# Performance work log

Measured on AMD Instinct MI355X. Metric: run time of the kernel, lower is better.

## Reference

```python
import jax, jax.numpy as jnp
import numpy as np

N = 100000      # nodes
E = 1600000     # edges (avg degree 16)
G = 2000        # graphs
D_IN = 4        # node_in_dim
H = 128         # hidden_dim
L = 3           # num_layers


def setup_inputs() -> dict:
    key = jax.random.key(0)
    ks = jax.random.split(key, 16)
    si = 1.0 / np.sqrt(D_IN)
    sh = 1.0 / np.sqrt(H)
    inp = {
        "x": jax.random.normal(ks[0], (N, D_IN), jnp.float32),
        "edge_index": jax.random.randint(ks[1], (2, E), 0, N, dtype=jnp.int32),
        "batch": jnp.sort(jax.random.randint(ks[2], (N,), 0, G, dtype=jnp.int32)),
        "proj_w": jax.random.normal(ks[3], (D_IN, H), jnp.float32) * si,
        "proj_b": jnp.zeros((H,), jnp.float32),
        "conv_w1": jax.random.normal(ks[4], (L, H, H), jnp.float32) * sh,
        "conv_b1": jnp.zeros((L, H), jnp.float32),
        "conv_w2": jax.random.normal(ks[5], (L, H, H), jnp.float32) * sh,
        "conv_b2": jnp.zeros((L, H), jnp.float32),
        "shared_w": jax.random.normal(ks[6], (H, H), jnp.float32) * sh,
        "shared_b": jnp.zeros((H,), jnp.float32),
        "e_w": jax.random.normal(ks[7], (H, 1), jnp.float32) * sh,
        "e_b": jnp.zeros((1,), jnp.float32),
        "d_w": jax.random.normal(ks[8], (H, 1), jnp.float32) * sh,
        "d_b": jnp.zeros((1,), jnp.float32),
    }
    return inp


def reference(x, edge_index, batch, proj_w, proj_b, conv_w1, conv_b1,
              conv_w2, conv_b2, shared_w, shared_b, e_w, e_b, d_w, d_b):
    src, dst = edge_index[0], edge_index[1]
    # input projection: [N, D_IN] -> [N, H]
    h = x @ proj_w + proj_b
    # GIN layers: h' = relu(MLP((1+eps)*h + sum_{j->i} h_j)), eps = 0
    for l in range(L):
        agg = jax.ops.segment_sum(h[src], dst, num_segments=N)  # scatter-add
        m = h + agg
        m = jax.nn.relu(m @ conv_w1[l] + conv_b1[l]) @ conv_w2[l] + conv_b2[l]
        h = jax.nn.relu(m)
    # global mean pool over graphs: [N, H] -> [G, H]
    sums = jax.ops.segment_sum(h, batch, num_segments=G)
    cnt = jax.ops.segment_sum(jnp.ones((N,), h.dtype), batch, num_segments=G)
    g = sums / jnp.maximum(cnt, 1.0)[:, None]
    # shared head (dropout inactive in eval)
    g = jax.nn.relu(g @ shared_w + shared_b)
    energy = (g @ e_w + e_b).reshape(-1)
    dipole = (g @ d_w + d_b).reshape(-1)
    return (energy, dipole)
```

## Files before the change

### kernel.cpp

```cpp
#include <hip/hip_runtime.h>
#include <hip/hip_bf16.h>

#define H 128
#define REGSZ 512
#define PCHUNK 4096

typedef short short8 __attribute__((ext_vector_type(8)));
typedef float f32x4 __attribute__((ext_vector_type(4)));

__device__ __forceinline__ float bf2f(unsigned short u) {
    union { unsigned int i; float f; } c; c.i = ((unsigned int)u) << 16; return c.f;
}
__device__ __forceinline__ unsigned short f2bf(float f) {
    return __builtin_bit_cast(unsigned short, __float2bfloat16(f));
}
__device__ __forceinline__ uint2 pack_fp8x8(const float* f) {
    unsigned int lo = 0, hi = 0;
    lo = __builtin_amdgcn_cvt_pk_fp8_f32(f[0], f[1], lo, 0);
    lo = __builtin_amdgcn_cvt_pk_fp8_f32(f[2], f[3], lo, 1);
    hi = __builtin_amdgcn_cvt_pk_fp8_f32(f[4], f[5], hi, 0);
    hi = __builtin_amdgcn_cvt_pk_fp8_f32(f[6], f[7], hi, 1);
    return make_uint2(lo, hi);
}
__device__ __forceinline__ void unpack_fp8x8(uint2 v, float* f) {
    f[0] = __builtin_amdgcn_cvt_f32_fp8(v.x, 0);
    f[1] = __builtin_amdgcn_cvt_f32_fp8(v.x, 1);
    f[2] = __builtin_amdgcn_cvt_f32_fp8(v.x, 2);
    f[3] = __builtin_amdgcn_cvt_f32_fp8(v.x, 3);
    f[4] = __builtin_amdgcn_cvt_f32_fp8(v.y, 0);
    f[5] = __builtin_amdgcn_cvt_f32_fp8(v.y, 1);
    f[6] = __builtin_amdgcn_cvt_f32_fp8(v.y, 2);
    f[7] = __builtin_amdgcn_cvt_f32_fp8(v.y, 3);
}

__global__ void proj_prep_kernel(const float* __restrict__ x, const float* __restrict__ pw,
                                 const float* __restrict__ pb, unsigned char* __restrict__ h8,
                                 int N, const float* __restrict__ cw1, const float* __restrict__ cw2,
                                 unsigned short* __restrict__ wt, int wtotal, int wblocks) {
    int b = blockIdx.x;
    int tid = threadIdx.x;
    if (b < wblocks) {
        int idx = b * 256 + tid;
        if (idx < wtotal) {
            int m = idx >> 14;
            int o = (idx >> 7) & 127;
            int i = idx & 127;
            const float* srcp = (m < 3) ? (cw1 + (size_t)m * H * H) : (cw2 + (size_t)(m - 3) * H * H);
            wt[idx] = f2bf(srcp[i * H + o]);
        }
        return;
    }
    int t2 = (b - wblocks) * 256 + tid;
    if (t2 >= N * 16) return;
    int i = t2 >> 4, c = (t2 & 15) * 8;
    float4 xv = *(const float4*)&x[i * 4];
    float acc[8];
#pragma unroll
    for (int j = 0; j < 8; ++j)
        acc[j] = pb[c + j] + xv.x * pw[0 * H + c + j] + xv.y * pw[1 * H + c + j]
               + xv.z * pw[2 * H + c + j] + xv.w * pw[3 * H + c + j];
    *(uint2*)&h8[(size_t)i * H + c] = pack_fp8x8(acc);
}

__global__ __launch_bounds__(256) void partition_kernel(
    const int* __restrict__ src, const int* __restrict__ dst,
    int* __restrict__ rcnt, int* __restrict__ bucket,
    int E, int nreg, int cap) {
    __shared__ int hcnt[256];
    __shared__ int hbase[256];
    int tid = threadIdx.x;
    hcnt[tid] = 0;
    __syncthreads();
    int e0 = blockIdx.x * PCHUNK;
    int e1 = min(e0 + PCHUNK, E);
    int nv = (e1 - e0) >> 2;
    const int4* dst4 = (const int4*)(dst + e0);
    const int4* src4 = (const int4*)(src + e0);
    for (int k = tid; k < nv; k += 256) {
        int4 d = dst4[k];
        atomicAdd(&hcnt[d.x >> 9], 1);
        atomicAdd(&hcnt[d.y >> 9], 1);
        atomicAdd(&hcnt[d.z >> 9], 1);
        atomicAdd(&hcnt[d.w >> 9], 1);
    }
    for (int e = e0 + (nv << 2) + tid; e < e1; e += 256)
        atomicAdd(&hcnt[dst[e] >> 9], 1);
    __syncthreads();
    {
        int c = hcnt[tid];
        hbase[tid] = (c > 0) ? atomicAdd(&rcnt[tid], c) : 0;
        hcnt[tid] = 0;
    }
    __syncthreads();
    for (int k = tid; k < nv; k += 256) {
        int4 d = dst4[k];
        int4 s = src4[k];
        int r, pos;
        r = d.x >> 9; pos = hbase[r] + atomicAdd(&hcnt[r], 1);
        if (pos < cap) bucket[(size_t)r * cap + pos] = ((d.x & (REGSZ - 1)) << 17) | s.x;
        r = d.y >> 9; pos = hbase[r] + atomicAdd(&hcnt[r], 1);
        if (pos < cap) bucket[(size_t)r * cap + pos] = ((d.y & (REGSZ - 1)) << 17) | s.y;
        r = d.z >> 9; pos = hbase[r] + atomicAdd(&hcnt[r], 1);
        if (pos < cap) bucket[(size_t)r * cap + pos] = ((d.z & (REGSZ - 1)) << 17) | s.z;
        r = d.w >> 9; pos = hbase[r] + atomicAdd(&hcnt[r], 1);
        if (pos < cap) bucket[(size_t)r * cap + pos] = ((d.w & (REGSZ - 1)) << 17) | s.w;
    }
    for (int e = e0 + (nv << 2) + tid; e < e1; e += 256) {
        int d = dst[e], s = src[e];
        int r = d >> 9;
        int pos = hbase[r] + atomicAdd(&hcnt[r], 1);
        if (pos < cap) bucket[(size_t)r * cap + pos] = ((d & (REGSZ - 1)) << 17) | s;
    }
}

__global__ __launch_bounds__(256) void csr_region_kernel(
    const int* __restrict__ rcnt, const int* __restrict__ bucket,
    int* __restrict__ offs, int* __restrict__ esrc,
    int N, int nreg, int cap) {
    __shared__ int cnt[REGSZ];
    __shared__ int part[256];
    __shared__ int sbase;
    int r = blockIdx.x;
    int tid = threadIdx.x;

    int v = (tid < nreg) ? rcnt[tid] : 0;
    part[tid] = v;
    __syncthreads();
    for (int off = 1; off < 256; off <<= 1) {
        int t = (tid >= off) ? part[tid - off] : 0;
        __syncthreads();
        part[tid] += t;
        __syncthreads();
    }
    if (tid == 0) sbase = (r == 0) ? 0 : part[r - 1];
    cnt[tid] = 0;
    cnt[tid + 256] = 0;
    __syncthreads();
    int base = sbase;
    int n = min(part[r] - base, cap);
    const int* bk = bucket + (size_t)r * cap;

    for (int p = tid; p < n; p += 256)
        atomicAdd(&cnt[bk[p] >> 17], 1);
    __syncthreads();

    int c0 = cnt[tid * 2], c1 = cnt[tid * 2 + 1];
    part[tid] = c0 + c1;
    __syncthreads();
    for (int off = 1; off < 256; off <<= 1) {
        int t = (tid >= off) ? part[tid - off] : 0;
        __syncthreads();
        part[tid] += t;
        __syncthreads();
    }
    int excl = (tid == 0) ? 0 : part[tid - 1];
    cnt[tid * 2] = excl;
    cnt[tid * 2 + 1] = excl + c0;
    __syncthreads();

    for (int p = tid; p < n; p += 256) {
        int e = bk[p];
        int pos = atomicAdd(&cnt[e >> 17], 1);
        esrc[base + pos] = e & 0x1FFFF;
    }
    __syncthreads();

    int lo = r * REGSZ;
#pragma unroll
    for (int i = tid; i < REGSZ; i += 256) {
        int node = lo + i;
        if (node < N) offs[node] = base + cnt[i];
    }
}

__global__ void gather_agg_kernel(const int* __restrict__ offs, const int* __restrict__ esrc,
                                  const unsigned char* __restrict__ h8, unsigned short* __restrict__ pre, int N) {
    int tid = blockIdx.x * 256 + threadIdx.x;
    if (tid >= N * 16) return;
    int node = tid >> 4, c = (tid & 15) * 8;
    int s = (node == 0) ? 0 : offs[node - 1];
    int e = offs[node];
    float acc[8];
    unpack_fp8x8(*(const uint2*)&h8[(size_t)node * H + c], acc);
    int i = s;
    for (; i + 3 < e; i += 4) {
        uint2 v[4];
#pragma unroll
        for (int k = 0; k < 4; ++k) v[k] = *(const uint2*)&h8[(size_t)esrc[i + k] * H + c];
#pragma unroll
        for (int k = 0; k < 4; ++k) {
            acc[0] += __builtin_amdgcn_cvt_f32_fp8(v[k].x, 0);
            acc[1] += __builtin_amdgcn_cvt_f32_fp8(v[k].x, 1);
            acc[2] += __builtin_amdgcn_cvt_f32_fp8(v[k].x, 2);
            acc[3] += __builtin_amdgcn_cvt_f32_fp8(v[k].x, 3);
            acc[4] += __builtin_amdgcn_cvt_f32_fp8(v[k].y, 0);
            acc[5] += __builtin_amdgcn_cvt_f32_fp8(v[k].y, 1);
            acc[6] += __builtin_amdgcn_cvt_f32_fp8(v[k].y, 2);
            acc[7] += __builtin_amdgcn_cvt_f32_fp8(v[k].y, 3);
        }
    }
    for (; i < e; ++i) {
        uint2 v = *(const uint2*)&h8[(size_t)esrc[i] * H + c];
        acc[0] += __builtin_amdgcn_cvt_f32_fp8(v.x, 0);
        acc[1] += __builtin_amdgcn_cvt_f32_fp8(v.x, 1);
        acc[2] += __builtin_amdgcn_cvt_f32_fp8(v.x, 2);
        acc[3] += __builtin_amdgcn_cvt_f32_fp8(v.x, 3);
        acc[4] += __builtin_amdgcn_cvt_f32_fp8(v.y, 0);
        acc[5] += __builtin_amdgcn_cvt_f32_fp8(v.y, 1);
        acc[6] += __builtin_amdgcn_cvt_f32_fp8(v.y, 2);
        acc[7] += __builtin_amdgcn_cvt_f32_fp8(v.y, 3);
    }
    short8 o;
#pragma unroll
    for (int j = 0; j < 8; ++j) o[j] = (short)f2bf(acc[j]);
    *(short8*)&pre[(size_t)node * H + c] = o;
}

template <bool LAST>
__global__ __launch_bounds__(1024) void fused_mlp_kernel(
    const unsigned short* __restrict__ pre,
    const unsigned short* __restrict__ W1t, const unsigned short* __restrict__ W2t,
    const float* __restrict__ b1, const float* __restrict__ b2,
    unsigned char* __restrict__ h8, const int* __restrict__ batch,
    float* __restrict__ gsum, int N) {
    __shared__ unsigned short As[256 * H];
    __shared__ unsigned short Ws1[H * H];
    __shared__ unsigned short Ws2[H * H];
    __shared__ int sbatch[256];
    int bm = blockIdx.x * 256;
    int tid = threadIdx.x;

#pragma unroll
    for (int rep = 0; rep < 4; ++rep) {
        int lin = rep * 1024 + tid;
        int r = lin >> 4, cb = lin & 15;
        int row = bm + r;
        short8 vv = {};
        if (row < N) vv = *(const short8*)&pre[(size_t)row * H + cb * 8];
        int byte = r * 256 + ((cb * 16) ^ ((r & 7) << 4));
        *(short8*)((char*)As + byte) = vv;
    }
#pragma unroll
    for (int rep = 0; rep < 2; ++rep) {
        int lin = rep * 1024 + tid;
        int o = lin >> 4, cb = lin & 15;
        int byte = o * 256 + ((cb * 16) ^ ((o & 7) << 4));
        *(short8*)((char*)Ws1 + byte) = *(const short8*)&W1t[(size_t)o * H + cb * 8];
        *(short8*)((char*)Ws2 + byte) = *(const short8*)&W2t[(size_t)o * H + cb * 8];
    }
    if (LAST && tid < 256) {
        int row = bm + tid;
        sbatch[tid] = (row < N) ? batch[row] : -1;
    }
    __syncthreads();

    int lane = tid & 63;
    int w = tid >> 6;
    int wr = (w >> 1) * 32;
    int wc = (w & 1) * 64;
    int lrow = lane & 15, kg = lane >> 4;

    float b1v[4], b2v[4];
#pragma unroll
    for (int ct = 0; ct < 4; ++ct) {
        b1v[ct] = b1[wc + ct * 16 + lrow];
        b2v[ct] = b2[wc + ct * 16 + lrow];
    }

    short8 a[2][4];
#pragma unroll
    for (int rt = 0; rt < 2; ++rt)
#pragma unroll
        for (int ks = 0; ks < 4; ++ks) {
            int r = wr + rt * 16 + lrow;
            int kb = ks * 64 + kg * 16;
            a[rt][ks] = *(short8*)((char*)As + r * 256 + (kb ^ ((r & 7) << 4)));
        }

    f32x4 acc[2][4] = {};
#pragma unroll
    for (int ct = 0; ct < 4; ++ct) {
#pragma unroll
        for (int ks = 0; ks < 4; ++ks) {
            int o = wc + ct * 16 + lrow;
            int kb = ks * 64 + kg * 16;
            short8 b = *(short8*)((char*)Ws1 + o * 256 + (kb ^ ((o & 7) << 4)));
            acc[0][ct] = __builtin_amdgcn_mfma_f32_16x16x32_bf16(a[0][ks], b, acc[0][ct], 0, 0, 0);
            acc[1][ct] = __builtin_amdgcn_mfma_f32_16x16x32_bf16(a[1][ks], b, acc[1][ct], 0, 0, 0);
        }
    }
    __syncthreads();

#pragma unroll
    for (int rt = 0; rt < 2; ++rt)
#pragma unroll
        for (int ct = 0; ct < 4; ++ct)
#pragma unroll
            for (int rr = 0; rr < 4; ++rr) {
                int r = wr + rt * 16 + kg * 4 + rr;
                int col = wc + ct * 16 + lrow;
                float v = fmaxf(acc[rt][ct][rr] + b1v[ct], 0.f);
                int byte = r * 256 + ((col * 2) ^ ((r & 7) << 4));
                *(unsigned short*)((char*)As + byte) = f2bf(v);
            }
    __syncthreads();

#pragma unroll
    for (int rt = 0; rt < 2; ++rt)
#pragma unroll
        for (int ks = 0; ks < 4; ++ks) {
            int r = wr + rt * 16 + lrow;
            int kb = ks * 64 + kg * 16;
            a[rt][ks] = *(short8*)((char*)As + r * 256 + (kb ^ ((r & 7) << 4)));
        }

    f32x4 acc2[2][4] = {};
#pragma unroll
    for (int ct = 0; ct < 4; ++ct) {
#pragma unroll
        for (int ks = 0; ks < 4; ++ks) {
            int o = wc + ct * 16 + lrow;
            int kb = ks * 64 + kg * 16;
            short8 b = *(short8*)((char*)Ws2 + o * 256 + (kb ^ ((o & 7) << 4)));
            acc2[0][ct] = __builtin_amdgcn_mfma_f32_16x16x32_bf16(a[0][ks], b, acc2[0][ct], 0, 0, 0);
            acc2[1][ct] = __builtin_amdgcn_mfma_f32_16x16x32_bf16(a[1][ks], b, acc2[1][ct], 0, 0, 0);
        }
    }
    __syncthreads();

#pragma unroll
    for (int rt = 0; rt < 2; ++rt)
#pragma unroll
        for (int ct = 0; ct < 4; ++ct)
#pragma unroll
            for (int rr = 0; rr < 4; ++rr) {
                int r = wr + rt * 16 + kg * 4 + rr;
                int col = wc + ct * 16 + lrow;
                float v = fmaxf(acc2[rt][ct][rr] + b2v[ct], 0.f);
                As[r * H + col] = f2bf(v);
            }
    __syncthreads();

    if (!LAST) {
#pragma unroll
        for (int rep = 0; rep < 4; ++rep) {
            int lin = rep * 1024 + tid;
            int r = lin >> 4, cb = lin & 15;
            int row = bm + r;
            if (row < N) {
                short8 v = *(short8*)&As[r * H + cb * 8];
                float f[8];
#pragma unroll
                for (int j = 0; j < 8; ++j) f[j] = bf2f((unsigned short)v[j]);
                *(uint2*)&h8[(size_t)row * H + cb * 8] = pack_fp8x8(f);
            }
        }
    } else {
        int col = tid & 127;
        int rg = tid >> 7;
        int r0 = rg * 32;
        int rmax = min(r0 + 32, N - bm);
        if (r0 < rmax) {
            float accp = 0.f;
            int cur = sbatch[r0];
            for (int r = r0; r < rmax; ++r) {
                int g = sbatch[r];
                if (g != cur) {
                    atomicAdd(&gsum[(size_t)cur * H + col], accp);
                    cur = g;
                    accp = 0.f;
                }
                accp += bf2f(As[r * H + col]);
            }
            atomicAdd(&gsum[(size_t)cur * H + col], accp);
        }
    }
}

__global__ __launch_bounds__(128) void head_kernel(
    const float* __restrict__ gsum, const int* __restrict__ batch,
    const float* __restrict__ sw, const float* __restrict__ sb,
    const float* __restrict__ ew, const float* __restrict__ eb,
    const float* __restrict__ dw, const float* __restrict__ db,
    float* __restrict__ out, int N, int G) {
    int g = blockIdx.x;
    int j = threadIdx.x;
    int s, e;
    {
        int lo = 0, hi = N;
        while (lo < hi) { int mid = (lo + hi) >> 1; if (batch[mid] < g) lo = mid + 1; else hi = mid; }
        s = lo;
        hi = N;
        while (lo < hi) { int mid = (lo + hi) >> 1; if (batch[mid] < g + 1) lo = mid + 1; else hi = mid; }
        e = lo;
    }
    float cnt = (float)(e - s);
    __shared__ float gm[H];
    gm[j] = gsum[(size_t)g * H + j] / fmaxf(cnt, 1.0f);
    __syncthreads();
    float t = sb[j];
    for (int k = 0; k < H; ++k) t += gm[k] * sw[k * H + j];
    t = fmaxf(t, 0.f);
    __shared__ float red[2][H];
    red[0][j] = t * ew[j];
    red[1][j] = t * dw[j];
    __syncthreads();
    for (int off = 64; off > 0; off >>= 1) {
        if (j < off) {
            red[0][j] += red[0][j + off];
            red[1][j] += red[1][j + off];
        }
        __syncthreads();
    }
    if (j == 0) {
        out[g] = red[0][0] + eb[0];
        out[G + g] = red[1][0] + db[0];
    }
}

extern "C" void kernel_launch(void* const* d_in, const int* in_sizes, int n_in,
                              void* d_out, int out_size, void* d_ws, size_t ws_size,
                              hipStream_t stream) {
    const float* x      = (const float*)d_in[0];
    const int*   ei     = (const int*)d_in[1];
    const int*   batch  = (const int*)d_in[2];
    const float* proj_w = (const float*)d_in[3];
    const float* proj_b = (const float*)d_in[4];
    const float* cw1    = (const float*)d_in[5];
    const float* cb1    = (const float*)d_in[6];
    const float* cw2    = (const float*)d_in[7];
    const float* cb2    = (const float*)d_in[8];
    const float* sw     = (const float*)d_in[9];
    const float* sb     = (const float*)d_in[10];
    const float* ew     = (const float*)d_in[11];
    const float* eb     = (const float*)d_in[12];
    const float* dw     = (const float*)d_in[13];
    const float* db     = (const float*)d_in[14];

    int N = in_sizes[0] / 4;
    int E = in_sizes[1] / 2;
    int G = out_size / 2;

    const int* src = ei;
    const int* dst = ei + E;

    unsigned short* pre = (unsigned short*)d_ws;
    unsigned short* wt  = pre + (size_t)N * H;
    int* offs  = (int*)(wt + 6 * H * H);
    int* rcnt  = offs + N + 1;
    float* gsum = (float*)(rcnt + 256);
    int* esrc  = (int*)(gsum + (size_t)G * H);
    unsigned char* h8 = (unsigned char*)(esrc + E);
    int* bucket = (int*)pre;

    float* out = (float*)d_out;

    int nreg = (N + REGSZ - 1) >> 9;
    int cap  = (E / nreg) * 5 / 4 + 1024;

    hipMemsetAsync(rcnt, 0, (256 + (size_t)G * H) * sizeof(int), stream);

    partition_kernel<<<(E + PCHUNK - 1) / PCHUNK, 256, 0, stream>>>(src, dst, rcnt, bucket, E, nreg, cap);
    csr_region_kernel<<<nreg, 256, 0, stream>>>(rcnt, bucket, offs, esrc, N, nreg, cap);

    int wtotal = 6 * H * H;
    int wblocks = (wtotal + 255) / 256;
    int pblocks = (N * 16 + 255) / 256;
    proj_prep_kernel<<<wblocks + pblocks, 256, 0, stream>>>(x, proj_w, proj_b, h8, N,
                                                            cw1, cw2, wt, wtotal, wblocks);

    int mlp_blocks = (N + 255) / 256;
    int gather_blocks = (N * 16 + 255) / 256;

    for (int l = 0; l < 3; ++l) {
        gather_agg_kernel<<<gather_blocks, 256, 0, stream>>>(offs, esrc, h8, pre, N);
        if (l < 2)
            fused_mlp_kernel<false><<<mlp_blocks, 1024, 0, stream>>>(
                pre, wt + (size_t)l * H * H, wt + (size_t)(3 + l) * H * H,
                cb1 + l * H, cb2 + l * H, h8, batch, gsum, N);
        else
            fused_mlp_kernel<true><<<mlp_blocks, 1024, 0, stream>>>(
                pre, wt + (size_t)l * H * H, wt + (size_t)(3 + l) * H * H,
                cb1 + l * H, cb2 + l * H, h8, batch, gsum, N);
    }

    head_kernel<<<G, 128, 0, stream>>>(gsum, batch, sw, sb, ew, eb, dw, db, out, N, G);
}
```

Before: 297.9 us.

## Merge partition and projection kernels; gather neighbours in source-range passes

```diff
diff --git a/kernel.cpp b/kernel.cpp
--- a/kernel.cpp
+++ b/kernel.cpp
@@ -33,12 +33,63 @@
     f[7] = __builtin_amdgcn_cvt_f32_fp8(v.y, 3);
 }
 
-__global__ void proj_prep_kernel(const float* __restrict__ x, const float* __restrict__ pw,
-                                 const float* __restrict__ pb, unsigned char* __restrict__ h8,
-                                 int N, const float* __restrict__ cw1, const float* __restrict__ cw2,
-                                 unsigned short* __restrict__ wt, int wtotal, int wblocks) {
+__global__ __launch_bounds__(256) void front_kernel(
+    const int* __restrict__ src, const int* __restrict__ dst,
+    int* __restrict__ rcnt, int* __restrict__ bucket, int E, int nreg, int cap, int pchunks,
+    const float* __restrict__ x, const float* __restrict__ pw, const float* __restrict__ pb,
+    unsigned char* __restrict__ h8, int N,
+    const float* __restrict__ cw1, const float* __restrict__ cw2,
+    unsigned short* __restrict__ wt, int wtotal, int wblocks) {
     int b = blockIdx.x;
     int tid = threadIdx.x;
+    if (b < pchunks) {
+        __shared__ int hcnt[256];
+        __shared__ int hbase[256];
+        hcnt[tid] = 0;
+        __syncthreads();
+        int e0 = b * PCHUNK;
+        int e1 = min(e0 + PCHUNK, E);
+        int nv = (e1 - e0) >> 2;
+        const int4* dst4 = (const int4*)(dst + e0);
+        const int4* src4 = (const int4*)(src + e0);
+        for (int k = tid; k < nv; k += 256) {
+            int4 d = dst4[k];
+            atomicAdd(&hcnt[d.x >> 9], 1);
+            atomicAdd(&hcnt[d.y >> 9], 1);
+            atomicAdd(&hcnt[d.z >> 9], 1);
+            atomicAdd(&hcnt[d.w >> 9], 1);
+        }
+        for (int e = e0 + (nv << 2) + tid; e < e1; e += 256)
+            atomicAdd(&hcnt[dst[e] >> 9], 1);
+        __syncthreads();
+        {
+            int c = hcnt[tid];
+            hbase[tid] = (c > 0) ? atomicAdd(&rcnt[tid], c) : 0;
+            hcnt[tid] = 0;
+        }
+        __syncthreads();
+        for (int k = tid; k < nv; k += 256) {
+            int4 d = dst4[k];
+            int4 s = src4[k];
+            int r, pos;
+            r = d.x >> 9; pos = hbase[r] + atomicAdd(&hcnt[r], 1);
+            if (pos < cap) bucket[(size_t)r * cap + pos] = ((d.x & (REGSZ - 1)) << 17) | s.x;
+            r = d.y >> 9; pos = hbase[r] + atomicAdd(&hcnt[r], 1);
+            if (pos < cap) bucket[(size_t)r * cap + pos] = ((d.y & (REGSZ - 1)) << 17) | s.y;
+            r = d.z >> 9; pos = hbase[r] + atomicAdd(&hcnt[r], 1);
+            if (pos < cap) bucket[(size_t)r * cap + pos] = ((d.z & (REGSZ - 1)) << 17) | s.z;
+            r = d.w >> 9; pos = hbase[r] + atomicAdd(&hcnt[r], 1);
+            if (pos < cap) bucket[(size_t)r * cap + pos] = ((d.w & (REGSZ - 1)) << 17) | s.w;
+        }
+        for (int e = e0 + (nv << 2) + tid; e < e1; e += 256) {
+            int d = dst[e], s = src[e];
+            int r = d >> 9;
+            int pos = hbase[r] + atomicAdd(&hcnt[r], 1);
+            if (pos < cap) bucket[(size_t)r * cap + pos] = ((d & (REGSZ - 1)) << 17) | s;
+        }
+        return;
+    }
+    b -= pchunks;
     if (b < wblocks) {
         int idx = b * 256 + tid;
         if (idx < wtotal) {
@@ -60,57 +111,6 @@
         acc[j] = pb[c + j] + xv.x * pw[0 * H + c + j] + xv.y * pw[1 * H + c + j]
                + xv.z * pw[2 * H + c + j] + xv.w * pw[3 * H + c + j];
     *(uint2*)&h8[(size_t)i * H + c] = pack_fp8x8(acc);
-}
-
-__global__ __launch_bounds__(256) void partition_kernel(
-    const int* __restrict__ src, const int* __restrict__ dst,
-    int* __restrict__ rcnt, int* __restrict__ bucket,
-    int E, int nreg, int cap) {
-    __shared__ int hcnt[256];
-    __shared__ int hbase[256];
-    int tid = threadIdx.x;
-    hcnt[tid] = 0;
-    __syncthreads();
-    int e0 = blockIdx.x * PCHUNK;
-    int e1 = min(e0 + PCHUNK, E);
-    int nv = (e1 - e0) >> 2;
-    const int4* dst4 = (const int4*)(dst + e0);
-    const int4* src4 = (const int4*)(src + e0);
-    for (int k = tid; k < nv; k += 256) {
-        int4 d = dst4[k];
-        atomicAdd(&hcnt[d.x >> 9], 1);
-        atomicAdd(&hcnt[d.y >> 9], 1);
-        atomicAdd(&hcnt[d.z >> 9], 1);
-        atomicAdd(&hcnt[d.w >> 9], 1);
-    }
-    for (int e = e0 + (nv << 2) + tid; e < e1; e += 256)
-        atomicAdd(&hcnt[dst[e] >> 9], 1);
-    __syncthreads();
-    {
-        int c = hcnt[tid];
-        hbase[tid] = (c > 0) ? atomicAdd(&rcnt[tid], c) : 0;
-        hcnt[tid] = 0;
-    }
-    __syncthreads();
-    for (int k = tid; k < nv; k += 256) {
-        int4 d = dst4[k];
-        int4 s = src4[k];
-        int r, pos;
-        r = d.x >> 9; pos = hbase[r] + atomicAdd(&hcnt[r], 1);
-        if (pos < cap) bucket[(size_t)r * cap + pos] = ((d.x & (REGSZ - 1)) << 17) | s.x;
-        r = d.y >> 9; pos = hbase[r] + atomicAdd(&hcnt[r], 1);
-        if (pos < cap) bucket[(size_t)r * cap + pos] = ((d.y & (REGSZ - 1)) << 17) | s.y;
-        r = d.z >> 9; pos = hbase[r] + atomicAdd(&hcnt[r], 1);
-        if (pos < cap) bucket[(size_t)r * cap + pos] = ((d.z & (REGSZ - 1)) << 17) | s.z;
-        r = d.w >> 9; pos = hbase[r] + atomicAdd(&hcnt[r], 1);
-        if (pos < cap) bucket[(size_t)r * cap + pos] = ((d.w & (REGSZ - 1)) << 17) | s.w;
-    }
-    for (int e = e0 + (nv << 2) + tid; e < e1; e += 256) {
-        int d = dst[e], s = src[e];
-        int r = d >> 9;
-        int pos = hbase[r] + atomicAdd(&hcnt[r], 1);
-        if (pos < cap) bucket[(size_t)r * cap + pos] = ((d & (REGSZ - 1)) << 17) | s;
-    }
 }
 
 __global__ __launch_bounds__(256) void csr_region_kernel(
@@ -182,33 +182,24 @@
     int e = offs[node];
     float acc[8];
     unpack_fp8x8(*(const uint2*)&h8[(size_t)node * H + c], acc);
-    int i = s;
-    for (; i + 3 < e; i += 4) {
-        uint2 v[4];
-#pragma unroll
-        for (int k = 0; k < 4; ++k) v[k] = *(const uint2*)&h8[(size_t)esrc[i + k] * H + c];
-#pragma unroll
-        for (int k = 0; k < 4; ++k) {
-            acc[0] += __builtin_amdgcn_cvt_f32_fp8(v[k].x, 0);
-            acc[1] += __builtin_amdgcn_cvt_f32_fp8(v[k].x, 1);
-            acc[2] += __builtin_amdgcn_cvt_f32_fp8(v[k].x, 2);
-            acc[3] += __builtin_amdgcn_cvt_f32_fp8(v[k].x, 3);
-            acc[4] += __builtin_amdgcn_cvt_f32_fp8(v[k].y, 0);
-            acc[5] += __builtin_amdgcn_cvt_f32_fp8(v[k].y, 1);
-            acc[6] += __builtin_amdgcn_cvt_f32_fp8(v[k].y, 2);
-            acc[7] += __builtin_amdgcn_cvt_f32_fp8(v[k].y, 3);
-        }
-    }
-    for (; i < e; ++i) {
-        uint2 v = *(const uint2*)&h8[(size_t)esrc[i] * H + c];
-        acc[0] += __builtin_amdgcn_cvt_f32_fp8(v.x, 0);
-        acc[1] += __builtin_amdgcn_cvt_f32_fp8(v.x, 1);
-        acc[2] += __builtin_amdgcn_cvt_f32_fp8(v.x, 2);
-        acc[3] += __builtin_amdgcn_cvt_f32_fp8(v.x, 3);
-        acc[4] += __builtin_amdgcn_cvt_f32_fp8(v.y, 0);
-        acc[5] += __builtin_amdgcn_cvt_f32_fp8(v.y, 1);
-        acc[6] += __builtin_amdgcn_cvt_f32_fp8(v.y, 2);
-        acc[7] += __builtin_amdgcn_cvt_f32_fp8(v.y, 3);
+    int qsz = (N + 3) >> 2;
+#pragma unroll
+    for (int p = 0; p < 4; ++p) {
+        int lo = p * qsz, hi = lo + qsz;
+        for (int i = s; i < e; ++i) {
+            int sidx = esrc[i];
+            if (sidx >= lo && sidx < hi) {
+                uint2 v = *(const uint2*)&h8[(size_t)sidx * H + c];
+                acc[0] += __builtin_amdgcn_cvt_f32_fp8(v.x, 0);
+                acc[1] += __builtin_amdgcn_cvt_f32_fp8(v.x, 1);
+                acc[2] += __builtin_amdgcn_cvt_f32_fp8(v.x, 2);
+                acc[3] += __builtin_amdgcn_cvt_f32_fp8(v.x, 3);
+                acc[4] += __builtin_amdgcn_cvt_f32_fp8(v.y, 0);
+                acc[5] += __builtin_amdgcn_cvt_f32_fp8(v.y, 1);
+                acc[6] += __builtin_amdgcn_cvt_f32_fp8(v.y, 2);
+                acc[7] += __builtin_amdgcn_cvt_f32_fp8(v.y, 3);
+            }
+        }
     }
     short8 o;
 #pragma unroll
@@ -460,14 +451,15 @@
 
     hipMemsetAsync(rcnt, 0, (256 + (size_t)G * H) * sizeof(int), stream);
 
-    partition_kernel<<<(E + PCHUNK - 1) / PCHUNK, 256, 0, stream>>>(src, dst, rcnt, bucket, E, nreg, cap);
-    csr_region_kernel<<<nreg, 256, 0, stream>>>(rcnt, bucket, offs, esrc, N, nreg, cap);
-
+    int pchunks = (E + PCHUNK - 1) / PCHUNK;
     int wtotal = 6 * H * H;
     int wblocks = (wtotal + 255) / 256;
     int pblocks = (N * 16 + 255) / 256;
-    proj_prep_kernel<<<wblocks + pblocks, 256, 0, stream>>>(x, proj_w, proj_b, h8, N,
-                                                            cw1, cw2, wt, wtotal, wblocks);
+    front_kernel<<<pchunks + wblocks + pblocks, 256, 0, stream>>>(
+        src, dst, rcnt, bucket, E, nreg, cap, pchunks,
+        x, proj_w, proj_b, h8, N, cw1, cw2, wt, wtotal, wblocks);
+
+    csr_region_kernel<<<nreg, 256, 0, stream>>>(rcnt, bucket, offs, esrc, N, nreg, cap);
 
     int mlp_blocks = (N + 255) / 256;
     int gather_blocks = (N * 16 + 255) / 256;
```

Result: slower. 653.9 us (+119.5%).
